# Optimization experiments

Hardware: AMD Instinct MI355X
Metric: run time of the kernel (lower is better)

## Reference

```python
import jax, jax.numpy as jnp
import numpy as np
import math

D_MODEL = 1024
N_HEAD = 16
HEAD_DIM = D_MODEL // N_HEAD


def setup_inputs() -> dict:
    key = jax.random.key(0)
    ks = jax.random.split(key, 9)
    B, S = 2, 2048
    x = jax.random.normal(ks[0], (B, S, D_MODEL), dtype=jnp.float32)
    # nn.Linear weights are [out, in]; default-ish init scale 0.02, phase projs std=0.005
    w = lambda k, std: jax.random.normal(k, (D_MODEL, D_MODEL), dtype=jnp.float32) * std
    return {
        "x": x,
        "Wq_amp": w(ks[1], 0.02),
        "Wk_amp": w(ks[2], 0.02),
        "Wq_phi": w(ks[3], 0.005),
        "Wk_phi": w(ks[4], 0.005),
        "Wv": w(ks[5], 0.02),
        "Wo": w(ks[6], 0.02),
        "score_log_scale": jnp.zeros((N_HEAD,), dtype=jnp.float32),
    }


def _split_heads(t):
    B, S, _ = t.shape
    return t.reshape(B, S, N_HEAD, HEAD_DIM).transpose(0, 2, 1, 3)  # [B,H,S,hd]


def reference(x, Wq_amp, Wk_amp, Wq_phi, Wk_phi, Wv, Wo, score_log_scale):
    B, S, _ = x.shape
    eps = 1e-6
    # amplitude (softplus) and phase (pi * tanh) projections
    q_amp = _split_heads(jax.nn.softplus(x @ Wq_amp.T))
    k_amp = _split_heads(jax.nn.softplus(x @ Wk_amp.T))
    q_phi = _split_heads(math.pi * jnp.tanh(x @ Wq_phi.T))
    k_phi = _split_heads(math.pi * jnp.tanh(x @ Wk_phi.T))
    # RMS-normalize amplitudes over head_dim
    q_amp = q_amp / jnp.sqrt(jnp.mean(q_amp * q_amp, axis=-1, keepdims=True) + eps)
    k_amp = k_amp / jnp.sqrt(jnp.mean(k_amp * k_amp, axis=-1, keepdims=True) + eps)
    # interference components
    q_cos = q_amp * jnp.cos(q_phi)
    q_sin = q_amp * jnp.sin(q_phi)
    k_cos = k_amp * jnp.cos(k_phi)
    k_sin = k_amp * jnp.sin(k_phi)
    # two-term score matmul, scaled
    scores = (jnp.einsum("bhqd,bhkd->bhqk", q_cos, k_cos)
              + jnp.einsum("bhqd,bhkd->bhqk", q_sin, k_sin)) / math.sqrt(HEAD_DIM)
    scores = scores * jnp.exp(score_log_scale)[None, :, None, None]
    # causal mask + softmax
    mask = jnp.tril(jnp.ones((S, S), dtype=bool))
    scores = jnp.where(mask[None, None], scores, -jnp.inf)
    attn = jax.nn.softmax(scores, axis=-1)
    v = _split_heads(x @ Wv.T)
    out = jnp.einsum("bhqk,bhkd->bhqd", attn, v)
    out = out.transpose(0, 2, 1, 3).reshape(B, S, D_MODEL)
    return out @ Wo.T
```

## Files before the change

kernel.cpp:

```cpp
#include <hip/hip_runtime.h>
#include <hip/hip_bf16.h>
#include <math.h>

#define S_LEN 2048
#define NH 16
#define HD 64
#define DM 1024
#define NTOK 4096
#define NBH 32

typedef __attribute__((ext_vector_type(8))) __bf16 bf16x8;
typedef __attribute__((ext_vector_type(8))) ushort ushort8;
typedef __attribute__((ext_vector_type(4))) ushort ushort4v;
typedef __attribute__((ext_vector_type(4))) float f32x4;
typedef __attribute__((ext_vector_type(16))) float f32x16;
typedef __attribute__((ext_vector_type(4))) uint u32x4;

__device__ __forceinline__ ushort f2b(float x) {
  __hip_bfloat16 h = __float2bfloat16(x);
  return *reinterpret_cast<ushort*>(&h);
}

__device__ __forceinline__ uint pk2(float lo, float hi) {
  return (uint)f2b(lo) | ((uint)f2b(hi) << 16);
}

#define EXP2(x) __builtin_amdgcn_exp2f(x)

__device__ __forceinline__ void gload16b(const void* g, void* l) {
  __builtin_amdgcn_global_load_lds((const __attribute__((address_space(1))) void*)g,
                                   (__attribute__((address_space(3))) void*)l, 16, 0, 0);
}

#define MFMA16(a, b, c) __builtin_amdgcn_mfma_f32_16x16x32_bf16((a), (b), (c), 0, 0, 0)
#define MFMA32(a, b, c) __builtin_amdgcn_mfma_f32_32x32x16_bf16((a), (b), (c), 0, 0, 0)

struct CvtArgs {
  const float* src[7];
  ushort* dst[7];
  int n[7];
};

__global__ void cvt_kernel(CvtArgs a) {
  int arr = blockIdx.y;
  const float* s = a.src[arr];
  ushort* d = a.dst[arr];
  long n = a.n[arr];
  for (long i = ((long)blockIdx.x * 256 + threadIdx.x) * 8; i < n; i += 512L * 256 * 8) {
    float4 v0 = *reinterpret_cast<const float4*>(s + i);
    float4 v1 = *reinterpret_cast<const float4*>(s + i + 4);
    ushort8 r;
    r[0] = f2b(v0.x); r[1] = f2b(v0.y); r[2] = f2b(v0.z); r[3] = f2b(v0.w);
    r[4] = f2b(v1.x); r[5] = f2b(v1.y); r[6] = f2b(v1.z); r[7] = f2b(v1.w);
    *reinterpret_cast<ushort8*>(d + i) = r;
  }
}

__global__ __launch_bounds__(256, 2) void qkproj_kernel(
    const ushort* __restrict__ A,
    const ushort* __restrict__ Wqa, const ushort* __restrict__ Wqp,
    const ushort* __restrict__ Wka, const ushort* __restrict__ Wkp,
    const ushort* __restrict__ Wv, const float* __restrict__ sls,
    ushort* __restrict__ qext, ushort* __restrict__ kext, ushort* __restrict__ vT) {
  __shared__ __align__(16) ushort Alds[3][4096];
  __shared__ __align__(16) ushort B0lds[3][4096];
  __shared__ __align__(16) ushort B1lds[3][4096];
  const int d = blockIdx.x;
  const int xc = d & 7, c = d >> 3;
  const int u = (c < 64) ? (xc * 64 + c) : (512 + xc * 32 + (c - 64));
  int z, bx, by;
  if (u < 512) { z = u >> 8; int v = u & 255; bx = v & 7; by = v >> 3; }
  else         { z = 2;      int v = u - 512; bx = v & 7; by = v >> 3; }
  const int t = threadIdx.x;
  const int lane = t & 63;
  const int wave = t >> 6;
  const int wm = wave >> 1, wn = wave & 1;
  const int l15 = lane & 15, g = lane >> 4;
  const int mbase = by * 128, nbase = bx * 128;
  const int K = DM;
  const int srow = t >> 2;
  const int sx = (srow >> 1) & 3;
  const int scol = (((t & 3) ^ sx)) * 8;
  const int xr = (l15 >> 1) & 3;
  const ushort* Ag = A + (size_t)(mbase + srow) * K + scol;
  const ushort* Wa = (z == 0) ? Wqa : (z == 1) ? Wka : Wv;
  const ushort* Wp = (z == 0) ? Wqp : Wkp;
  const ushort* Wag = Wa + (size_t)(nbase + srow) * K + scol;
  const ushort* Wpg = (z < 2) ? (Wp + (size_t)(nbase + srow) * K + scol) : Wag;

  const int nk = K / 32;
  f32x4 accA[4][4] = {};

  if (z < 2) {
    f32x4 accP[4][4] = {};
    auto stage = [&](int buf, int kt) {
      gload16b(Ag + kt, &Alds[buf][t * 8]);
      gload16b(Ag + kt + (size_t)64 * K, &Alds[buf][t * 8 + 64 * 32]);
      gload16b(Wag + kt, &B0lds[buf][t * 8]);
      gload16b(Wag + kt + (size_t)64 * K, &B0lds[buf][t * 8 + 64 * 32]);
      gload16b(Wpg + kt, &B1lds[buf][t * 8]);
      gload16b(Wpg + kt + (size_t)64 * K, &B1lds[buf][t * 8 + 64 * 32]);
    };
    stage(0, 0);
    stage(1, 32);
    int cur = 0;
    for (int kt = 0; kt < nk; ++kt) {
      if (kt + 2 < nk) {
        int b2 = cur + 2; if (b2 >= 3) b2 -= 3;
        stage(b2, (kt + 2) * 32);
        asm volatile("s_waitcnt vmcnt(12)" ::: "memory");
      } else if (kt + 1 < nk) {
        asm volatile("s_waitcnt vmcnt(6)" ::: "memory");
      } else {
        asm volatile("s_waitcnt vmcnt(0)" ::: "memory");
      }
      __builtin_amdgcn_s_barrier();
      bf16x8 af[4], ba[4], bp[4];
#pragma unroll
      for (int i = 0; i < 4; i++)
        af[i] = *reinterpret_cast<const bf16x8*>(
            &Alds[cur][(wm * 64 + i * 16 + l15) * 32 + (g ^ xr) * 8]);
#pragma unroll
      for (int j = 0; j < 4; j++) {
        ba[j] = *reinterpret_cast<const bf16x8*>(
            &B0lds[cur][(wn * 64 + j * 16 + l15) * 32 + (g ^ xr) * 8]);
        bp[j] = *reinterpret_cast<const bf16x8*>(
            &B1lds[cur][(wn * 64 + j * 16 + l15) * 32 + (g ^ xr) * 8]);
      }
      __builtin_amdgcn_s_setprio(1);
#pragma unroll
      for (int i = 0; i < 4; i++)
#pragma unroll
        for (int j = 0; j < 4; j++) {
          accA[i][j] = MFMA16(af[i], ba[j], accA[i][j]);
          accP[i][j] = MFMA16(af[i], bp[j], accP[i][j]);
        }
      __builtin_amdgcn_s_setprio(0);
      __builtin_amdgcn_s_barrier();
      cur = (cur + 1 == 3) ? 0 : cur + 1;
    }
    const int row0 = mbase + wm * 64;
    const int h = (nbase >> 6) + wn;
    const float scale = (z == 0) ? __expf(sls[h]) * 0.125f * 1.44269504f : 1.0f;
    ushort* ext = (z == 0) ? qext : kext;
#pragma unroll
    for (int i = 0; i < 4; i++) {
#pragma unroll
      for (int r = 0; r < 4; r++) {
        float sp[4];
        float ss = 0.0f;
#pragma unroll
        for (int j = 0; j < 4; j++) {
          float v = accA[i][j][r];
          sp[j] = fmaxf(v, 0.0f) + __logf(1.0f + __expf(-fabsf(v)));
          ss += sp[j] * sp[j];
        }
        ss += __shfl_xor(ss, 1);
        ss += __shfl_xor(ss, 2);
        ss += __shfl_xor(ss, 4);
        ss += __shfl_xor(ss, 8);
        float rn = rsqrtf(ss * (1.0f / 64.0f) + 1e-6f) * scale;
        const int token = row0 + i * 16 + g * 4 + r;
        const int bb = token >> 11, sidx = token & 2047;
        ushort* base = ext + (((size_t)(bb * NH + h) * S_LEN + sidx) << 7);
#pragma unroll
        for (int j = 0; j < 4; j++) {
          float e = __expf(2.0f * accP[i][j][r]);
          float th = 1.0f - 2.0f * __builtin_amdgcn_rcpf(e + 1.0f);
          float phi = 3.14159265358979f * th;
          float sn = __sinf(phi), cs = __cosf(phi);
          float a = sp[j] * rn;
          int dd = j * 16 + l15;
          base[dd] = f2b(a * cs);
          base[64 + dd] = f2b(a * sn);
        }
      }
    }
  } else {
    auto stage = [&](int buf, int kt) {
      gload16b(Ag + kt, &Alds[buf][t * 8]);
      gload16b(Ag + kt + (size_t)64 * K, &Alds[buf][t * 8 + 64 * 32]);
      gload16b(Wag + kt, &B0lds[buf][t * 8]);
      gload16b(Wag + kt + (size_t)64 * K, &B0lds[buf][t * 8 + 64 * 32]);
    };
    stage(0, 0);
    stage(1, 32);
    int cur = 0;
    for (int kt = 0; kt < nk; ++kt) {
      if (kt + 2 < nk) {
        int b2 = cur + 2; if (b2 >= 3) b2 -= 3;
        stage(b2, (kt + 2) * 32);
        asm volatile("s_waitcnt vmcnt(8)" ::: "memory");
      } else if (kt + 1 < nk) {
        asm volatile("s_waitcnt vmcnt(4)" ::: "memory");
      } else {
        asm volatile("s_waitcnt vmcnt(0)" ::: "memory");
      }
      __builtin_amdgcn_s_barrier();
      bf16x8 af[4], ba[4];
#pragma unroll
      for (int i = 0; i < 4; i++)
        af[i] = *reinterpret_cast<const bf16x8*>(
            &Alds[cur][(wm * 64 + i * 16 + l15) * 32 + (g ^ xr) * 8]);
#pragma unroll
      for (int j = 0; j < 4; j++)
        ba[j] = *reinterpret_cast<const bf16x8*>(
            &B0lds[cur][(wn * 64 + j * 16 + l15) * 32 + (g ^ xr) * 8]);
      __builtin_amdgcn_s_setprio(1);
#pragma unroll
      for (int i = 0; i < 4; i++)
#pragma unroll
        for (int j = 0; j < 4; j++)
          accA[i][j] = MFMA16(af[i], ba[j], accA[i][j]);
      __builtin_amdgcn_s_setprio(0);
      __builtin_amdgcn_s_barrier();
      cur = (cur + 1 == 3) ? 0 : cur + 1;
    }
    const int row0 = mbase + wm * 64, col0 = nbase + wn * 64;
#pragma unroll
    for (int i = 0; i < 4; i++)
#pragma unroll
      for (int j = 0; j < 4; j++) {
        int col = col0 + j * 16 + l15;
        int h = col >> 6, hd = col & 63;
        int t0 = row0 + i * 16 + g * 4;
        int bb = t0 >> 11, s0 = t0 & 2047;
        ushort4v w;
#pragma unroll
        for (int r = 0; r < 4; r++) w[r] = f2b(accA[i][j][r]);
        *reinterpret_cast<ushort4v*>(
            &vT[(((size_t)(bb * NH + h) * HD + hd) << 11) + s0]) = w;
      }
  }
}

__global__ __launch_bounds__(256) void gemm_bt(const ushort* __restrict__ A,
                                               const ushort* __restrict__ W,
                                               float* __restrict__ Cout,
                                               int M, int N, int K) {
  __shared__ __align__(16) ushort Alds[4][4096];
  __shared__ __align__(16) ushort Blds[4][4096];
  const int d = blockIdx.x;
  const int u = (d & 7) * 32 + (d >> 3);
  const int bx = u & 7, by = u >> 3;
  const int t = threadIdx.x;
  const int lane = t & 63;
  const int wave = t >> 6;
  const int wm = wave >> 1, wn = wave & 1;
  const int l15 = lane & 15, g = lane >> 4;
  const int mbase = by * 128, nbase = bx * 128;
  const int srow = t >> 2;
  const int sx = (srow >> 1) & 3;
  const int scol = (((t & 3) ^ sx)) * 8;
  const int xr = (l15 >> 1) & 3;
  const ushort* Ag = A + (size_t)(mbase + srow) * K + scol;
  const ushort* Wg = W + (size_t)(nbase + srow) * K + scol;
  auto stage = [&](int buf, int kt) {
    gload16b(Ag + kt, &Alds[buf][t * 8]);
    gload16b(Ag + kt + (size_t)64 * K, &Alds[buf][t * 8 + 64 * 32]);
    gload16b(Wg + kt, &Blds[buf][t * 8]);
    gload16b(Wg + kt + (size_t)64 * K, &Blds[buf][t * 8 + 64 * 32]);
  };
  const int nk = K / 32;
  stage(0, 0);
  stage(1, 32);
  stage(2, 64);
  f32x4 acc[4][4] = {};
  for (int kt = 0; kt < nk; ++kt) {
    const int cur = kt & 3;
    if (kt + 3 < nk) {
      stage((cur + 3) & 3, (kt + 3) * 32);
      asm volatile("s_waitcnt vmcnt(12)" ::: "memory");
    } else if (kt + 2 < nk) {
      asm volatile("s_waitcnt vmcnt(8)" ::: "memory");
    } else if (kt + 1 < nk) {
      asm volatile("s_waitcnt vmcnt(4)" ::: "memory");
    } else {
      asm volatile("s_waitcnt vmcnt(0)" ::: "memory");
    }
    __builtin_amdgcn_s_barrier();
    bf16x8 af[4], bfr[4];
#pragma unroll
    for (int i = 0; i < 4; i++)
      af[i] = *reinterpret_cast<const bf16x8*>(
          &Alds[cur][(wm * 64 + i * 16 + l15) * 32 + (g ^ xr) * 8]);
#pragma unroll
    for (int j = 0; j < 4; j++)
      bfr[j] = *reinterpret_cast<const bf16x8*>(
          &Blds[cur][(wn * 64 + j * 16 + l15) * 32 + (g ^ xr) * 8]);
    __builtin_amdgcn_s_setprio(1);
#pragma unroll
    for (int i = 0; i < 4; i++)
#pragma unroll
      for (int j = 0; j < 4; j++)
        acc[i][j] = MFMA16(af[i], bfr[j], acc[i][j]);
    __builtin_amdgcn_s_setprio(0);
    __builtin_amdgcn_s_barrier();
  }
  const int row0 = mbase + wm * 64, col0 = nbase + wn * 64;
#pragma unroll
  for (int i = 0; i < 4; i++)
#pragma unroll
    for (int j = 0; j < 4; j++)
#pragma unroll
      for (int r = 0; r < 4; r++) {
        int row = row0 + i * 16 + g * 4 + r;
        int col = col0 + j * 16 + l15;
        Cout[(size_t)row * N + col] = acc[i][j][r];
      }
}

__device__ __forceinline__ void stage_kv(const char* Kp, const char* Vp, int kb,
                                         char* buf, int wave, int lane) {
#pragma unroll
  for (int c = 0; c < 4; c++) {
    int i = wave * 4 + c;
    int kvl = i * 4 + (lane >> 4);
    int slot = (lane & 15) ^ (kvl & 7);
    gload16b(Kp + (size_t)(kb + kvl) * 256 + slot * 16, buf + i * 1024);
  }
#pragma unroll
  for (int c = 0; c < 2; c++) {
    int i = wave * 2 + c;
    int hd = i * 8 + (lane >> 3);
    int slot = (lane & 7) ^ (hd & 7);
    gload16b(Vp + (size_t)hd * (S_LEN * 2) + (size_t)kb * 2 + slot * 16,
             buf + 16384 + i * 1024);
  }
}

__global__ __launch_bounds__(256, 3) void attn_kernel(const ushort* __restrict__ qext,
                                                      const ushort* __restrict__ kext,
                                                      const ushort* __restrict__ vT,
                                                      ushort* __restrict__ attnout,
                                                      float* __restrict__ part) {
  __shared__ __align__(16) char lds[2][24576];
  const int d = blockIdx.x;
  const int xcd = d & 7, c = d >> 3;
  const int bh = xcd * 4 + (c & 3);
  const int w = c >> 2;
  int qt, t0, t1, half;
  bool split;
  if (w < 8) { qt = w; t0 = 0; t1 = 2 * qt + 1; split = false; half = 0; }
  else {
    int ww = w - 8;
    qt = 8 + (ww >> 1); half = ww & 1; split = true;
    if (half == 0) { t0 = 0; t1 = qt; } else { t0 = qt + 1; t1 = 2 * qt + 1; }
  }
  const int b = bh >> 4, h = bh & 15;
  const int wave = threadIdx.x >> 6, lane = threadIdx.x & 63;
  const int l31 = lane & 31, hi = lane >> 5;
  const int qb = qt * 128;
  const int qw = qb + wave * 32;
  const int qa = qw + l31;
  const char* Kp = (const char*)(kext + (size_t)bh * S_LEN * 128);
  const char* Vp = (const char*)(vT + (size_t)bh * HD * S_LEN);
  const ushort* Qp = qext + (size_t)bh * S_LEN * 128;
  const int ksw = l31 & 7;

  stage_kv(Kp, Vp, t0 << 6, lds[0], wave, lane);
  bf16x8 qf[8];
#pragma unroll
  for (int s = 0; s < 8; s++)
    qf[s] = *reinterpret_cast<const bf16x8*>(&Qp[(size_t)qa * 128 + s * 16 + hi * 8]);

  f32x16 o0 = {}, o1 = {};
  float m = -1e30f, ls = 0.0f;

  for (int t = t0; t <= t1; ++t) {
    const int cur = (t - t0) & 1;
    const int kb = t << 6;
    if (t < t1) {
      stage_kv(Kp, Vp, (t + 1) << 6, lds[cur ^ 1], wave, lane);
      asm volatile("s_waitcnt vmcnt(6)" ::: "memory");
    } else {
      asm volatile("s_waitcnt vmcnt(0)" ::: "memory");
    }
    __builtin_amdgcn_s_barrier();

    const char* Kb = lds[cur];
    const char* Vb = lds[cur] + 16384;

    f32x16 st0 = {}, st1 = {};
    __builtin_amdgcn_s_setprio(1);
#pragma unroll
    for (int s = 0; s < 8; s++) {
      int sl = ((s * 2 + hi) ^ ksw) << 4;
      bf16x8 k0 = *(const bf16x8*)(Kb + l31 * 256 + sl);
      bf16x8 k1 = *(const bf16x8*)(Kb + (32 + l31) * 256 + sl);
      st0 = MFMA32(k0, qf[s], st0);
      st1 = MFMA32(k1, qf[s], st1);
    }
    __builtin_amdgcn_s_setprio(0);

    if (kb + 64 > qw) {
#pragma unroll
      for (int r = 0; r < 16; r++) {
        int kv = kb + (r & 3) + 8 * (r >> 2) + 4 * hi;
        if (kv > qa) st0[r] = -1e30f;
        if (kv + 32 > qa) st1[r] = -1e30f;
      }
    }
    float pm = -1e30f;
#pragma unroll
    for (int r = 0; r < 16; r++) pm = fmaxf(pm, fmaxf(st0[r], st1[r]));
    pm = fmaxf(pm, __shfl_xor(pm, 32));
    if (!__all(pm <= m + 11.5416f)) {
      float mn = fmaxf(m, pm);
      float corr = EXP2(m - mn);
      m = mn;
      ls *= corr;
#pragma unroll
      for (int r = 0; r < 16; r++) { o0[r] *= corr; o1[r] *= corr; }
    }
    float ssum = 0.0f;
#pragma unroll
    for (int r = 0; r < 16; r++) {
      st0[r] = EXP2(st0[r] - m);
      st1[r] = EXP2(st1[r] - m);
      ssum += st0[r] + st1[r];
    }
    ssum += __shfl_xor(ssum, 32);
    ls += ssum;

    u32x4 pb[4];
#pragma unroll
    for (int hf = 0; hf < 2; hf++) {
      const f32x16& st = hf ? st1 : st0;
      uint cA0 = pk2(st[0], st[1]),  cA1 = pk2(st[2], st[3]);
      uint cB0 = pk2(st[4], st[5]),  cB1 = pk2(st[6], st[7]);
      uint cC0 = pk2(st[8], st[9]),  cC1 = pk2(st[10], st[11]);
      uint cD0 = pk2(st[12], st[13]), cD1 = pk2(st[14], st[15]);
      uint xA0 = __shfl_xor(cA0, 32), xA1 = __shfl_xor(cA1, 32);
      uint xB0 = __shfl_xor(cB0, 32), xB1 = __shfl_xor(cB1, 32);
      uint xC0 = __shfl_xor(cC0, 32), xC1 = __shfl_xor(cC1, 32);
      uint xD0 = __shfl_xor(cD0, 32), xD1 = __shfl_xor(cD1, 32);
      u32x4 lo, hi4;
      lo[0] = cA0; lo[1] = cA1; lo[2] = xA0; lo[3] = xA1;
      hi4[0] = xB0; hi4[1] = xB1; hi4[2] = cB0; hi4[3] = cB1;
      pb[hf * 2] = hi ? hi4 : lo;
      u32x4 lo2, hi2;
      lo2[0] = cC0; lo2[1] = cC1; lo2[2] = xC0; lo2[3] = xC1;
      hi2[0] = xD0; hi2[1] = xD1; hi2[2] = cD0; hi2[3] = cD1;
      pb[hf * 2 + 1] = hi ? hi2 : lo2;
    }
    __builtin_amdgcn_s_setprio(1);
#pragma unroll
    for (int ks = 0; ks < 4; ks++) {
      int sl = ((ks * 2 + hi) ^ ksw) << 4;
      bf16x8 v0 = *(const bf16x8*)(Vb + l31 * 128 + sl);
      bf16x8 v1 = *(const bf16x8*)(Vb + (32 + l31) * 128 + sl);
      bf16x8 pbb = *reinterpret_cast<const bf16x8*>(&pb[ks]);
      o0 = MFMA32(v0, pbb, o0);
      o1 = MFMA32(v1, pbb, o1);
    }
    __builtin_amdgcn_s_setprio(0);
    __builtin_amdgcn_s_barrier();
  }

  if (!split) {
    float inv = 1.0f / ls;
    ushort* Op = attnout + ((size_t)b * S_LEN + qa) * DM + h * HD;
#pragma unroll
    for (int g4 = 0; g4 < 4; g4++) {
      ushort4v w0, w1;
#pragma unroll
      for (int jj = 0; jj < 4; jj++) {
        w0[jj] = f2b(o0[4 * g4 + jj] * inv);
        w1[jj] = f2b(o1[4 * g4 + jj] * inv);
      }
      *reinterpret_cast<ushort4v*>(Op + 8 * g4 + 4 * hi) = w0;
      *reinterpret_cast<ushort4v*>(Op + 32 + 8 * g4 + 4 * hi) = w1;
    }
  } else {
    float* P = part + ((size_t)(half * 256 + bh * 8 + (qt - 8)) * 128
                       + (wave * 32 + l31)) * 72;
#pragma unroll
    for (int g4 = 0; g4 < 4; g4++) {
      float4 a0 = make_float4(o0[4 * g4], o0[4 * g4 + 1], o0[4 * g4 + 2], o0[4 * g4 + 3]);
      float4 a1 = make_float4(o1[4 * g4], o1[4 * g4 + 1], o1[4 * g4 + 2], o1[4 * g4 + 3]);
      *reinterpret_cast<float4*>(P + 8 * g4 + 4 * hi) = a0;
      *reinterpret_cast<float4*>(P + 32 + 8 * g4 + 4 * hi) = a1;
    }
    if (hi == 0) { P[64] = m; P[65] = ls; }
  }
}

__global__ void attn_merge(const float* __restrict__ part, ushort* __restrict__ attnout) {
  const int blk = blockIdx.x;
  const int row = threadIdx.x;
  const int bh = blk >> 3, qt = (blk & 7) + 8;
  const float* Pa = part + ((size_t)blk * 128 + row) * 72;
  const float* Pb = part + ((size_t)(256 + blk) * 128 + row) * 72;
  float mA = Pa[64], lsA = Pa[65], mB = Pb[64], lsB = Pb[65];
  float M = fmaxf(mA, mB);
  float ca = EXP2(mA - M), cb = EXP2(mB - M);
  float inv = 1.0f / (lsA * ca + lsB * cb);
  const int b = bh >> 4, h = bh & 15;
  const int q = qt * 128 + row;
  ushort* Op = attnout + ((size_t)b * S_LEN + q) * DM + h * HD;
#pragma unroll
  for (int dd = 0; dd < 64; dd += 4) {
    float4 va = *reinterpret_cast<const float4*>(Pa + dd);
    float4 vb = *reinterpret_cast<const float4*>(Pb + dd);
    ushort4v wv;
    wv[0] = f2b((va.x * ca + vb.x * cb) * inv);
    wv[1] = f2b((va.y * ca + vb.y * cb) * inv);
    wv[2] = f2b((va.z * ca + vb.z * cb) * inv);
    wv[3] = f2b((va.w * ca + vb.w * cb) * inv);
    *reinterpret_cast<ushort4v*>(Op + dd) = wv;
  }
}

extern "C" void kernel_launch(void* const* d_in, const int* in_sizes, int n_in,
                              void* d_out, int out_size, void* d_ws, size_t ws_size,
                              hipStream_t stream) {
  const float* x   = (const float*)d_in[0];
  const float* Wqa = (const float*)d_in[1];
  const float* Wka = (const float*)d_in[2];
  const float* Wqp = (const float*)d_in[3];
  const float* Wkp = (const float*)d_in[4];
  const float* Wv  = (const float*)d_in[5];
  const float* Wo  = (const float*)d_in[6];
  const float* sls = (const float*)d_in[7];

  char* ws = (char*)d_ws;
  ushort* x_bf = (ushort*)ws; ws += (size_t)NTOK * DM * 2;
  ushort* w_bf[6];
  for (int i = 0; i < 6; i++) { w_bf[i] = (ushort*)ws; ws += (size_t)DM * DM * 2; }
  ushort* qext = (ushort*)ws; ws += (size_t)NBH * S_LEN * 128 * 2;
  ushort* kext = (ushort*)ws; ws += (size_t)NBH * S_LEN * 128 * 2;
  ushort* vT   = (ushort*)ws; ws += (size_t)NBH * HD * S_LEN * 2;
  ushort* attn = (ushort*)ws; ws += (size_t)NTOK * DM * 2;
  float* part  = (float*)ws;  ws += (size_t)2 * 256 * 128 * 72 * 4;

  CvtArgs ca;
  ca.src[0] = x; ca.dst[0] = x_bf; ca.n[0] = NTOK * DM;
  const float* wsrc[6] = {Wqa, Wka, Wqp, Wkp, Wv, Wo};
  for (int i = 0; i < 6; i++) { ca.src[i + 1] = wsrc[i]; ca.dst[i + 1] = w_bf[i]; ca.n[i + 1] = DM * DM; }
  hipLaunchKernelGGL(cvt_kernel, dim3(512, 7), dim3(256), 0, stream, ca);

  hipLaunchKernelGGL(qkproj_kernel, dim3(768), dim3(256), 0, stream,
                     x_bf, w_bf[0], w_bf[2], w_bf[1], w_bf[3], w_bf[4], sls,
                     qext, kext, vT);

  hipLaunchKernelGGL(attn_kernel, dim3(768), dim3(256), 0, stream,
                     qext, kext, vT, attn, part);
  hipLaunchKernelGGL(attn_merge, dim3(256), dim3(128), 0, stream, part, attn);

  hipLaunchKernelGGL(gemm_bt, dim3(256), dim3(256), 0, stream, attn, w_bf[5],
                     (float*)d_out, NTOK, DM, DM);
}
```

Measured before the change: 154.0 us.

## Switch QK projection GEMM to double-buffered LDS with three blocks per CU

Cuts the LDS staging buffers in the QK/V projection kernel from three to two. The next stage is now issued after the second barrier, and the waitcnt thresholds are adjusted to match. The smaller LDS footprint, together with launch_bounds raised to 3, is meant to let more blocks share a CU and hide latency. The trade-off is a shallower prefetch pipeline and possible register pressure or spills under the tighter launch bound.

```diff
diff --git a/kernel.cpp b/kernel.cpp
--- a/kernel.cpp
+++ b/kernel.cpp
@@ -56,15 +56,15 @@
   }
 }
 
-__global__ __launch_bounds__(256, 2) void qkproj_kernel(
+__global__ __launch_bounds__(256, 3) void qkproj_kernel(
     const ushort* __restrict__ A,
     const ushort* __restrict__ Wqa, const ushort* __restrict__ Wqp,
     const ushort* __restrict__ Wka, const ushort* __restrict__ Wkp,
     const ushort* __restrict__ Wv, const float* __restrict__ sls,
     ushort* __restrict__ qext, ushort* __restrict__ kext, ushort* __restrict__ vT) {
-  __shared__ __align__(16) ushort Alds[3][4096];
-  __shared__ __align__(16) ushort B0lds[3][4096];
-  __shared__ __align__(16) ushort B1lds[3][4096];
+  __shared__ __align__(16) ushort Alds[2][4096];
+  __shared__ __align__(16) ushort B0lds[2][4096];
+  __shared__ __align__(16) ushort B1lds[2][4096];
   const int d = blockIdx.x;
   const int xc = d & 7, c = d >> 3;
   const int u = (c < 64) ? (xc * 64 + c) : (512 + xc * 32 + (c - 64));
@@ -103,17 +103,10 @@
     };
     stage(0, 0);
     stage(1, 32);
-    int cur = 0;
     for (int kt = 0; kt < nk; ++kt) {
-      if (kt + 2 < nk) {
-        int b2 = cur + 2; if (b2 >= 3) b2 -= 3;
-        stage(b2, (kt + 2) * 32);
-        asm volatile("s_waitcnt vmcnt(12)" ::: "memory");
-      } else if (kt + 1 < nk) {
-        asm volatile("s_waitcnt vmcnt(6)" ::: "memory");
-      } else {
-        asm volatile("s_waitcnt vmcnt(0)" ::: "memory");
-      }
+      const int cur = kt & 1;
+      if (kt + 1 < nk) asm volatile("s_waitcnt vmcnt(6)" ::: "memory");
+      else             asm volatile("s_waitcnt vmcnt(0)" ::: "memory");
       __builtin_amdgcn_s_barrier();
       bf16x8 af[4], ba[4], bp[4];
 #pragma unroll
@@ -137,7 +130,7 @@
         }
       __builtin_amdgcn_s_setprio(0);
       __builtin_amdgcn_s_barrier();
-      cur = (cur + 1 == 3) ? 0 : cur + 1;
+      if (kt + 2 < nk) stage(cur, (kt + 2) * 32);
     }
     const int row0 = mbase + wm * 64;
     const int h = (nbase >> 6) + wn;
@@ -185,17 +178,10 @@
     };
     stage(0, 0);
     stage(1, 32);
-    int cur = 0;
     for (int kt = 0; kt < nk; ++kt) {
-      if (kt + 2 < nk) {
-        int b2 = cur + 2; if (b2 >= 3) b2 -= 3;
-        stage(b2, (kt + 2) * 32);
-        asm volatile("s_waitcnt vmcnt(8)" ::: "memory");
-      } else if (kt + 1 < nk) {
-        asm volatile("s_waitcnt vmcnt(4)" ::: "memory");
-      } else {
-        asm volatile("s_waitcnt vmcnt(0)" ::: "memory");
-      }
+      const int cur = kt & 1;
+      if (kt + 1 < nk) asm volatile("s_waitcnt vmcnt(4)" ::: "memory");
+      else             asm volatile("s_waitcnt vmcnt(0)" ::: "memory");
       __builtin_amdgcn_s_barrier();
       bf16x8 af[4], ba[4];
 #pragma unroll
@@ -214,7 +200,7 @@
           accA[i][j] = MFMA16(af[i], ba[j], accA[i][j]);
       __builtin_amdgcn_s_setprio(0);
       __builtin_amdgcn_s_barrier();
-      cur = (cur + 1 == 3) ? 0 : cur + 1;
+      if (kt + 2 < nk) stage(cur, (kt + 2) * 32);
     }
     const int row0 = mbase + wm * 64, col0 = nbase + wn * 64;
 #pragma unroll
```

Result: slower. 208.0 us (+35.1%).
